# Optimization experiments

Measured on AMD Instinct MI355X. Metric: run time of the kernel, lower is better.

Reference implementation:

```python
import jax, jax.numpy as jnp
import numpy as np

B, T, IN, HID, BR, OUT = 128, 250, 700, 1024, 4, 20
VTH1, VTH2, DT = 0.5, 0.5, 1.0

# heaviside spike with multi-gaussian surrogate grad (DH-SNN ActFun_adp)
@jax.custom_vjp
def spike_fn(v):
    return (v > 0).astype(v.dtype)

def _spike_fwd(v):
    return spike_fn(v), v

def _spike_bwd(v, g):
    gamma, lens, scale, hight = 0.5, 0.5, 6.0, 0.15
    def gauss(x, mu, sigma):
        return jnp.exp(-((x - mu) ** 2) / (2.0 * sigma ** 2)) / (jnp.sqrt(2.0 * jnp.pi) * sigma)
    sg = (gauss(v, 0.0, lens) * (1.0 + hight)
          - gauss(v, lens, scale * lens) * hight
          - gauss(v, -lens, scale * lens) * hight)
    return (g * sg * gamma,)

spike_fn.defvjp(_spike_fwd, _spike_bwd)

def _make_mask(rng):
    # each output neuron's BR branches see disjoint equal slices of a random permutation
    K = IN + HID  # pad == 0 since (IN+HID) % BR == 0
    seg = K // BR
    mask = np.zeros((HID * BR, K), dtype=np.int32)
    for i in range(HID):
        seq = rng.permutation(K)
        for j in range(BR):
            mask[i * BR + j, seq[j * seg:(j + 1) * seg]] = 1
    return mask

def setup_inputs() -> dict:
    key = jax.random.key(0)
    ks = jax.random.split(key, 10)
    K = IN + HID
    x = jax.random.uniform(ks[0], (B, T, IN), dtype=jnp.float32)
    W1 = jax.random.normal(ks[1], (HID * BR, K), dtype=jnp.float32) / jnp.sqrt(jnp.float32(K))
    b1 = jnp.zeros((HID * BR,), jnp.float32)
    tau_m1 = jax.random.uniform(ks[2], (HID,), jnp.float32, 0.0, 4.0)
    tau_n = jax.random.uniform(ks[3], (HID, BR), jnp.float32, 0.0, 4.0)
    W2 = jax.random.normal(ks[4], (OUT, HID), dtype=jnp.float32) / jnp.sqrt(jnp.float32(HID))
    b2 = jnp.zeros((OUT,), jnp.float32)
    tau_m2 = jax.random.uniform(ks[5], (OUT,), jnp.float32, 0.0, 4.0)
    mem1_0 = jax.random.uniform(ks[6], (B, HID), jnp.float32)
    mem2_0 = jax.random.uniform(ks[7], (B, OUT), jnp.float32)
    mask = jnp.asarray(_make_mask(np.random.default_rng(0)))
    return dict(x=x, W1=W1, b1=b1, tau_m1=tau_m1, tau_n=tau_n, W2=W2, b2=b2,
                tau_m2=tau_m2, mem1_0=mem1_0, mem2_0=mem2_0, mask=mask)

def reference(x, W1, b1, tau_m1, tau_n, W2, b2, tau_m2, mem1_0, mem2_0, mask):
    bsz = x.shape[0]
    W1m = W1 * mask.astype(W1.dtype)  # branch-sparse dendritic weights
    alpha1 = jax.nn.sigmoid(tau_m1)   # [HID]
    beta = jax.nn.sigmoid(tau_n)      # [HID, BR]
    alpha2 = jax.nn.sigmoid(tau_m2)   # [OUT]
    spk1_0 = jnp.zeros((bsz, HID), x.dtype)
    d0 = jnp.zeros((bsz, HID, BR), x.dtype)
    spk2_0 = jnp.zeros((bsz, OUT), x.dtype)

    def step(carry, x_t):
        mem1, spk1, d_inp, mem2, spk2 = carry
        k_in = jnp.concatenate([x_t, spk1], axis=1)          # [B, IN+HID]
        ff = (k_in @ W1m.T + b1).reshape(bsz, HID, BR)       # dendritic branch input
        d_inp = beta * d_inp + (1.0 - beta) * ff             # per-branch decay
        l_in = d_inp.sum(axis=2)                             # [B, HID]
        mem1 = mem1 * alpha1 + (1.0 - alpha1) * l_in - VTH1 * spk1 * DT
        spk1 = spike_fn(mem1 - VTH1)
        d2 = spk1 @ W2.T + b2
        mem2 = mem2 * alpha2 + (1.0 - alpha2) * d2 - VTH2 * spk2 * DT
        spk2 = spike_fn(mem2 - VTH2)
        out = jax.nn.log_softmax(mem2, axis=1)
        return (mem1, spk1, d_inp, mem2, spk2), out

    _, ys = jax.lax.scan(step, (mem1_0, spk1_0, d0, mem2_0, spk2_0), jnp.swapaxes(x, 0, 1))
    return jnp.transpose(ys, (1, 2, 0))  # [B, OUT, T]
```

## Files before the change

### kernel.cpp

```cpp
#include <hip/hip_runtime.h>
#include <stdint.h>

#define BATCH 128
#define TSTEPS 250
#define NIN 700
#define NHID 1024
#define NBR 4
#define NOUT 20
#define KDIM 1724
#define NR 4096
#define VTH 0.5f


__global__ void setup_small(const float* __restrict__ tau_m1, const float* __restrict__ tau_n,
                            const float* __restrict__ tau_m2, const float* __restrict__ W2,
                            float* __restrict__ alpha1, float* __restrict__ beta,
                            float* __restrict__ alpha2, float* __restrict__ W2T) {
    int i = blockIdx.x * blockDim.x + threadIdx.x;
    if (i < NHID)  alpha1[i] = 1.f / (1.f + expf(-tau_m1[i]));
    if (i < NR)    beta[i]   = 1.f / (1.f + expf(-tau_n[i]));
    if (i < 32)    alpha2[i] = (i < NOUT) ? 1.f / (1.f + expf(-tau_m2[i])) : 0.f;
    if (i < NHID * 32) {
        int j = i >> 5, o = i & 31;
        W2T[i] = (o < NOUT) ? W2[o * NHID + j] : 0.f;
    }
}

__global__ void setup_weights(const float* __restrict__ W1, const int* __restrict__ mask,
                              float* __restrict__ W1xT, float* __restrict__ W1hTb) {
    const int total1 = NIN * NR;
    const int total2 = 256 * 16384;
    for (int i = blockIdx.x * blockDim.x + threadIdx.x; i < total1 + total2;
         i += gridDim.x * blockDim.x) {
        if (i < total1) {
            int k = i >> 12, r = i & 4095;
            size_t src = (size_t)r * KDIM + k;
            W1xT[i] = W1[src] * (float)mask[src];
        } else {
            int j = i - total1;
            int blk = j >> 14, rem = j & 16383;
            int n = rem >> 4, rl = rem & 15;
            int r = (blk << 4) + rl;
            size_t src = (size_t)r * KDIM + NIN + n;
            W1hTb[j] = W1[src] * (float)mask[src];
        }
    }
}

__global__ void init_state(const float* __restrict__ mem1_0, const float* __restrict__ mem2_0,
                           float* __restrict__ mem1, float* __restrict__ mem2,
                           float* __restrict__ spk2, float* __restrict__ d_inp,
                           uint32_t* __restrict__ spkg, uint32_t* __restrict__ cnt) {
    int i = blockIdx.x * blockDim.x + threadIdx.x;
    if (i < BATCH * NR) d_inp[i] = 0.f;
    if (i < BATCH * NHID) mem1[i] = mem1_0[i];
    if (i < BATCH * NOUT) { mem2[i] = mem2_0[i]; spk2[i] = 0.f; }
    if (i < 8192) spkg[i] = 0u;
    if (i == 0) cnt[0] = 0u;
}


#define GBM 128
#define GBN 128
#define GBK 16

__global__ __launch_bounds__(256) void ffx_gemm(const float* __restrict__ x,
                                                const float* __restrict__ W1xT,
                                                const float* __restrict__ b1,
                                                float* __restrict__ ffx, int t0) {
    __shared__ float As[GBK][GBM];
    __shared__ float Bs[GBK][GBN];
    int dt = blockIdx.x, bn = blockIdx.y;
    int tid = threadIdx.x;
    int tn = tid & 15, tm = tid >> 4;

    float acc[8][8];
#pragma unroll
    for (int i = 0; i < 8; ++i)
#pragma unroll
        for (int j = 0; j < 8; ++j) acc[i][j] = 0.f;

    int m_l = tid >> 1;
    const float* xrow = x + ((size_t)m_l * TSTEPS + t0 + dt) * NIN;
    int kh = (tid & 1) * 8;
    int kb = tid >> 4;
    int nb = (tid & 15) * 8;

    for (int k0 = 0; k0 < NIN; k0 += GBK) {
        float av[8];
#pragma unroll
        for (int u = 0; u < 8; ++u) {
            int k = k0 + kh + u;
            av[u] = (k < NIN) ? xrow[k] : 0.f;
        }
#pragma unroll
        for (int u = 0; u < 8; ++u) As[kh + u][m_l] = av[u];

        bool kok = (k0 + kb) < NIN;
        const float* bp = W1xT + (size_t)(k0 + kb) * NR + bn * GBN + nb;
        float bv[8];
#pragma unroll
        for (int u = 0; u < 8; ++u) bv[u] = kok ? bp[u] : 0.f;
#pragma unroll
        for (int u = 0; u < 8; ++u) Bs[kb][nb + u] = bv[u];

        __syncthreads();
#pragma unroll
        for (int kk = 0; kk < GBK; ++kk) {
            float a[8], b[8];
#pragma unroll
            for (int u = 0; u < 8; ++u) a[u] = As[kk][tm * 8 + u];
#pragma unroll
            for (int u = 0; u < 8; ++u) b[u] = Bs[kk][tn * 8 + u];
#pragma unroll
            for (int i = 0; i < 8; ++i)
#pragma unroll
                for (int j = 0; j < 8; ++j) acc[i][j] += a[i] * b[j];
        }
        __syncthreads();
    }

    float bias[8];
#pragma unroll
    for (int j = 0; j < 8; ++j) bias[j] = b1[bn * GBN + tn * 8 + j];
#pragma unroll
    for (int i = 0; i < 8; ++i) {
        int brow = tm * 8 + i;
        float* cp = ffx + ((size_t)dt * BATCH + brow) * NR + bn * GBN + tn * 8;
#pragma unroll
        for (int j = 0; j < 8; ++j) cp[j] = acc[i][j] + bias[j];
    }
}


__global__ __launch_bounds__(1024) void persist2(
    const float* __restrict__ alpha1, const float* __restrict__ beta,
    const float* __restrict__ alpha2, float* __restrict__ mem1,
    float* __restrict__ mem2, float* __restrict__ spk2,
    float* __restrict__ d_inp, const float* __restrict__ W1hTb,
    const float* __restrict__ W2T, const float* __restrict__ ffx,
    const float* __restrict__ b2v, float* __restrict__ out,
    uint32_t* __restrict__ spkg, uint32_t* __restrict__ cnt,
    int t0, int tc, int last, int epoch0) {
    __shared__ float lds_W[NHID * 17];
    __shared__ uint32_t lds_spk[4096];
    __shared__ uint32_t lds_mask[128 * 33];

    const int blk = blockIdx.x;
    const int tid = threadIdx.x;

    {
        const float4* wsrc = (const float4*)(W1hTb + (size_t)blk * 16384);
        for (int i4 = tid; i4 < 4096; i4 += 1024) {
            float4 v = wsrc[i4];
            int n = i4 >> 2, rb = (i4 & 3) * 4;
            lds_W[n * 17 + rb + 0] = v.x;
            lds_W[n * 17 + rb + 1] = v.y;
            lds_W[n * 17 + rb + 2] = v.z;
            lds_W[n * 17 + rb + 3] = v.w;
        }
    }

    const int r_l = tid & 15;
    const int bg  = tid >> 4;
    const int r_g = (blk << 4) + r_l;
    const int neuron = (blk << 2) + (r_l >> 2);
    const float beta_r = beta[r_g];
    const float al = alpha1[neuron];
    const int b0 = bg * 2, b1 = bg * 2 + 1;

    float di0 = d_inp[(size_t)b0 * NR + r_g];
    float di1 = d_inp[(size_t)b1 * NR + r_g];
    float mm0 = mem1[b0 * NHID + neuron];
    float mm1 = mem1[b1 * NHID + neuron];

    const int o2 = tid & 31;
    const int sub = tid >> 5;
    const bool l2blk = (blk < 16) && ((sub & 3) == 0);
    const int b2b = (blk << 3) + (sub >> 2);
    float m2 = 0.f, s2v = 0.f, a2 = 0.f, bo = 0.f;
    if (l2blk && o2 < NOUT) {
        a2 = alpha2[o2];
        bo = b2v[o2];
        m2 = mem2[b2b * NOUT + o2];
        s2v = spk2[b2b * NOUT + o2];
    }

    const int iters = tc + (last ? 1 : 0);
    for (int it = 0; it < iters; ++it) {
        const int tt = t0 + it;

        float ff0 = 0.f, ff1 = 0.f;
        if (tt < TSTEPS) {
            const float* fr = ffx + (size_t)it * ((size_t)BATCH * NR);
            ff0 = fr[(size_t)b0 * NR + r_g];
            ff1 = fr[(size_t)b1 * NR + r_g];
        }

        {
            const uint32_t* spg = spkg + (size_t)((tt + 1) & 1) * 4096;
#pragma unroll
            for (int k = 0; k < 4; ++k) {
                int idx = tid + (k << 10);
                lds_spk[idx ^ ((idx >> 7) & 31)] =
                    __hip_atomic_load(&spg[idx], __ATOMIC_RELAXED, __HIP_MEMORY_SCOPE_AGENT);
            }
        }
        __syncthreads();

        {
            const int w = tid & 31;
            const int bq = tid >> 5;
            const int g = bq >> 1;
            uint32_t sw[8];
#pragma unroll
            for (int m = 0; m < 8; ++m) {
                int raw = (w << 7) + (m << 4) + g;
                sw[m] = lds_spk[raw ^ (w & 31)];
            }
#pragma unroll
            for (int u = 0; u < 4; ++u) {
                const int b = (bq << 2) + u;
                const int j = ((bq & 1) << 2) + u;
                uint32_t word = 0;
#pragma unroll
                for (int m = 0; m < 8; ++m)
                    word |= ((sw[m] >> (j << 2)) & 0xFu) << (m << 2);
                lds_mask[b * 33 + w] = word;
            }
        }
        __syncthreads();

        uint32_t* spn = spkg + (size_t)(tt & 1) * 4096;

        if (tt < TSTEPS) {
            const uint32_t* mw0 = &lds_mask[b0 * 33];
            const uint32_t* mw1 = &lds_mask[b1 * 33];
            float acc0 = 0.f, acc1 = 0.f;
            for (int w = 0; w < 32; ++w) {
                uint32_t bits0 = mw0[w];
                while (bits0) {
                    int p = __builtin_ctz(bits0);
                    bits0 &= bits0 - 1;
                    acc0 += lds_W[((w << 5) + p) * 17 + r_l];
                }
                uint32_t bits1 = mw1[w];
                while (bits1) {
                    int p = __builtin_ctz(bits1);
                    bits1 &= bits1 - 1;
                    acc1 += lds_W[((w << 5) + p) * 17 + r_l];
                }
            }
            di0 = beta_r * di0 + (1.f - beta_r) * (acc0 + ff0);
            di1 = beta_r * di1 + (1.f - beta_r) * (acc1 + ff1);
            float ls0 = di0 + __shfl_xor(di0, 1); ls0 += __shfl_xor(ls0, 2);
            float ls1 = di1 + __shfl_xor(di1, 1); ls1 += __shfl_xor(ls1, 2);
            float sp0 = (float)((mw0[neuron >> 5] >> (neuron & 31)) & 1u);
            float sp1 = (float)((mw1[neuron >> 5] >> (neuron & 31)) & 1u);
            float mn0 = mm0 * al + (1.f - al) * ls0 - VTH * sp0;  mm0 = mn0;
            float mn1 = mm1 * al + (1.f - al) * ls1 - VTH * sp1;  mm1 = mn1;
            bool sk0 = (mn0 - VTH) > 0.f;
            bool sk1 = (mn1 - VTH) > 0.f;
            unsigned long long bal0 = __ballot(sk0 && ((r_l & 3) == 0));
            unsigned long long bal1 = __ballot(sk1 && ((r_l & 3) == 0));
            uint32_t dw = 0;
#pragma unroll
            for (int q = 0; q < 4; ++q) {
                uint32_t nb0 = (uint32_t)((bal0 >> (q * 16)) & 1ull)
                             | ((uint32_t)((bal0 >> (q * 16 + 4)) & 1ull) << 1)
                             | ((uint32_t)((bal0 >> (q * 16 + 8)) & 1ull) << 2)
                             | ((uint32_t)((bal0 >> (q * 16 + 12)) & 1ull) << 3);
                uint32_t nb1 = (uint32_t)((bal1 >> (q * 16)) & 1ull)
                             | ((uint32_t)((bal1 >> (q * 16 + 4)) & 1ull) << 1)
                             | ((uint32_t)((bal1 >> (q * 16 + 8)) & 1ull) << 2)
                             | ((uint32_t)((bal1 >> (q * 16 + 12)) & 1ull) << 3);
                dw |= (nb0 << (q * 8)) | (nb1 << (q * 8 + 4));
            }
            if ((tid & 63) == 0)
                __hip_atomic_store(&spn[(blk << 4) + (tid >> 6)], dw, __ATOMIC_RELAXED,
                                   __HIP_MEMORY_SCOPE_AGENT);
        }

        if (tt > 0 && l2blk) {
            const uint32_t* mw = &lds_mask[b2b * 33];
            float d2 = bo;
            for (int w = 0; w < 32; ++w) {
                uint32_t bits = mw[w];
                while (bits) {
                    int p = __builtin_ctz(bits);
                    bits &= bits - 1;
                    d2 += W2T[(((w << 5) + p) << 5) + o2];
                }
            }
            float m2n = m2 * a2 + (1.f - a2) * d2 - VTH * s2v;
            m2 = m2n;
            s2v = ((m2n - VTH) > 0.f) ? 1.f : 0.f;
            float v = (o2 < NOUT) ? m2n : -3.4e38f;
#pragma unroll
            for (int off = 16; off >= 1; off >>= 1) v = fmaxf(v, __shfl_xor(v, off, 32));
            float e = (o2 < NOUT) ? expf(m2n - v) : 0.f;
            float s = e;
#pragma unroll
            for (int off = 16; off >= 1; off >>= 1) s += __shfl_xor(s, off, 32);
            if (o2 < NOUT) out[((size_t)b2b * NOUT + o2) * TSTEPS + (tt - 1)] = (m2n - v) - logf(s);
        }

        if (it + 1 < iters) {
            __syncthreads();
            if (tid == 0) {
                __hip_atomic_fetch_add(cnt, 1u, __ATOMIC_RELEASE, __HIP_MEMORY_SCOPE_AGENT);
                uint32_t tgt = 256u * (uint32_t)(epoch0 + it + 1);
                while (__hip_atomic_load(cnt, __ATOMIC_RELAXED, __HIP_MEMORY_SCOPE_AGENT) < tgt)
                    __builtin_amdgcn_s_sleep(2);
            }
            __syncthreads();
        }
    }

    d_inp[(size_t)b0 * NR + r_g] = di0;
    d_inp[(size_t)b1 * NR + r_g] = di1;
    if ((r_l & 3) == 0) {
        mem1[b0 * NHID + neuron] = mm0;
        mem1[b1 * NHID + neuron] = mm1;
    }
    if (l2blk && o2 < NOUT) {
        mem2[b2b * NOUT + o2] = m2;
        spk2[b2b * NOUT + o2] = s2v;
    }
}


extern "C" void kernel_launch(void* const* d_in, const int* in_sizes, int n_in,
                              void* d_out, int out_size, void* d_ws, size_t ws_size,
                              hipStream_t stream) {
    const float* x      = (const float*)d_in[0];
    const float* W1     = (const float*)d_in[1];
    const float* b1     = (const float*)d_in[2];
    const float* tau_m1 = (const float*)d_in[3];
    const float* tau_n  = (const float*)d_in[4];
    const float* W2     = (const float*)d_in[5];
    const float* b2     = (const float*)d_in[6];
    const float* tau_m2 = (const float*)d_in[7];
    const float* mem1_0 = (const float*)d_in[8];
    const float* mem2_0 = (const float*)d_in[9];
    const int*   mask   = (const int*)d_in[10];
    float* out = (float*)d_out;

    float* ws = (float*)d_ws;
    size_t F = 0;
    float* alpha1 = ws + F; F += 1024;
    float* beta   = ws + F; F += 4096;
    float* alpha2 = ws + F; F += 32;
    float* mem1   = ws + F; F += BATCH * NHID;
    float* mem2   = ws + F; F += BATCH * NOUT;
    float* spk2   = ws + F; F += BATCH * NOUT;
    float* d_inp  = ws + F; F += BATCH * NR;
    float* W1xT   = ws + F; F += (size_t)NIN * NR;
    float* W1hTb  = ws + F; F += (size_t)256 * 16384;
    float* W2T    = ws + F; F += NHID * 32;
    uint32_t* spkg = (uint32_t*)(ws + F); F += 2 * BATCH * 64;
    uint32_t* cnt  = (uint32_t*)(ws + F); F += 64;
    float* ffx = ws + F;

    size_t ws_f = ws_size / 4;
    size_t avail = (ws_f > F) ? (ws_f - F) : 0;
    size_t per_t = (size_t)BATCH * NR;
    int Tc = (int)(avail / per_t);
    if (Tc < 1) Tc = 1;
    if (Tc > TSTEPS) Tc = TSTEPS;

    hipLaunchKernelGGL(setup_small, dim3(128), dim3(256), 0, stream,
                       tau_m1, tau_n, tau_m2, W2, alpha1, beta, alpha2, W2T);
    hipLaunchKernelGGL(setup_weights, dim3(2048), dim3(256), 0, stream, W1, mask, W1xT, W1hTb);
    hipLaunchKernelGGL(init_state, dim3(2048), dim3(256), 0, stream,
                       mem1_0, mem2_0, mem1, mem2, spk2, d_inp, spkg, cnt);

    int chunk_start = 0;
    int barriers_done = 0;
    while (chunk_start < TSTEPS) {
        int tc = TSTEPS - chunk_start;
        if (tc > Tc) tc = Tc;
        int last = (chunk_start + tc >= TSTEPS) ? 1 : 0;

        hipLaunchKernelGGL(ffx_gemm, dim3(tc, 32), dim3(256), 0, stream,
                           x, W1xT, b1, ffx, chunk_start);
        hipLaunchKernelGGL(persist2, dim3(256), dim3(1024), 0, stream,
                           alpha1, beta, alpha2, mem1, mem2, spk2, d_inp, W1hTb, W2T,
                           ffx, b2, out, spkg, cnt, chunk_start, tc, last, barriers_done);

        int iters = tc + (last ? 1 : 0);
        barriers_done += iters - 1;
        chunk_start += tc;
    }
}
```

Baseline: 7.089 ms.

## Replace global counter barrier with per-timestep per-block spike flags

The single atomic-counter grid barrier between timesteps is replaced by per-timestep, per-block ready flags with release/acquire semantics. Spike words now go into a per-timestep buffer rather than a double buffer, so each block waits only until all 256 producer flags for its step are set and never spins on one contended counter. The layer-2 readout is also split across 32 blocks with an 8-way partial-sum reduction in LDS, replacing 16 blocks that each did a serial loop. This costs more workspace for the spike and flag arrays and adds extra __syncthreads inside the step loop.

```diff
diff --git a/kernel.cpp b/kernel.cpp
--- a/kernel.cpp
+++ b/kernel.cpp
@@ -50,13 +50,13 @@
 __global__ void init_state(const float* __restrict__ mem1_0, const float* __restrict__ mem2_0,
                            float* __restrict__ mem1, float* __restrict__ mem2,
                            float* __restrict__ spk2, float* __restrict__ d_inp,
-                           uint32_t* __restrict__ spkg, uint32_t* __restrict__ cnt) {
+                           uint32_t* __restrict__ spkdat, uint32_t* __restrict__ spkseq) {
     int i = blockIdx.x * blockDim.x + threadIdx.x;
     if (i < BATCH * NR) d_inp[i] = 0.f;
     if (i < BATCH * NHID) mem1[i] = mem1_0[i];
     if (i < BATCH * NOUT) { mem2[i] = mem2_0[i]; spk2[i] = 0.f; }
-    if (i < 8192) spkg[i] = 0u;
-    if (i == 0) cnt[0] = 0u;
+    if (i < 4096) spkdat[i] = 0u;
+    if (i < (TSTEPS + 1) * 256) spkseq[i] = (i < 256) ? 1u : 0u;
 }
 
 
@@ -133,15 +133,15 @@
 }
 
 
-__global__ __launch_bounds__(1024) void persist2(
+__global__ __launch_bounds__(1024) void persist3(
     const float* __restrict__ alpha1, const float* __restrict__ beta,
     const float* __restrict__ alpha2, float* __restrict__ mem1,
     float* __restrict__ mem2, float* __restrict__ spk2,
     float* __restrict__ d_inp, const float* __restrict__ W1hTb,
     const float* __restrict__ W2T, const float* __restrict__ ffx,
     const float* __restrict__ b2v, float* __restrict__ out,
-    uint32_t* __restrict__ spkg, uint32_t* __restrict__ cnt,
-    int t0, int tc, int last, int epoch0) {
+    uint32_t* __restrict__ spkdat, uint32_t* __restrict__ spkseq,
+    int t0, int tc, int last) {
     __shared__ float lds_W[NHID * 17];
     __shared__ uint32_t lds_spk[4096];
     __shared__ uint32_t lds_mask[128 * 33];
@@ -176,19 +176,30 @@
 
     const int o2 = tid & 31;
     const int sub = tid >> 5;
-    const bool l2blk = (blk < 16) && ((sub & 3) == 0);
-    const int b2b = (blk << 3) + (sub >> 2);
+    const bool l2red = (blk < 32) && ((sub & 7) == 0);
+    const int b2b = (blk << 2) + (sub >> 3);
     float m2 = 0.f, s2v = 0.f, a2 = 0.f, bo = 0.f;
-    if (l2blk && o2 < NOUT) {
+    if (l2red && o2 < NOUT) {
         a2 = alpha2[o2];
         bo = b2v[o2];
         m2 = mem2[b2b * NOUT + o2];
         s2v = spk2[b2b * NOUT + o2];
     }
+    float* lds_f = (float*)lds_spk;
 
     const int iters = tc + (last ? 1 : 0);
     for (int it = 0; it < iters; ++it) {
         const int tt = t0 + it;
+
+        {
+            const uint32_t* fl = spkseq + (size_t)tt * 256;
+            if (tid < 256) {
+                while (__hip_atomic_load(fl + tid, __ATOMIC_ACQUIRE,
+                                         __HIP_MEMORY_SCOPE_AGENT) == 0u)
+                    __builtin_amdgcn_s_sleep(1);
+            }
+            __syncthreads();
+        }
 
         float ff0 = 0.f, ff1 = 0.f;
         if (tt < TSTEPS) {
@@ -198,7 +209,7 @@
         }
 
         {
-            const uint32_t* spg = spkg + (size_t)((tt + 1) & 1) * 4096;
+            const uint32_t* spg = spkdat + (size_t)tt * 4096;
 #pragma unroll
             for (int k = 0; k < 4; ++k) {
                 int idx = tid + (k << 10);
@@ -231,9 +242,8 @@
         }
         __syncthreads();
 
-        uint32_t* spn = spkg + (size_t)(tt & 1) * 4096;
-
         if (tt < TSTEPS) {
+            uint32_t* spn = spkdat + (size_t)(tt + 1) * 4096;
             const uint32_t* mw0 = &lds_mask[b0 * 33];
             const uint32_t* mw1 = &lds_mask[b1 * 33];
             float acc0 = 0.f, acc1 = 0.f;
@@ -281,17 +291,32 @@
                                    __HIP_MEMORY_SCOPE_AGENT);
         }
 
-        if (tt > 0 && l2blk) {
-            const uint32_t* mw = &lds_mask[b2b * 33];
-            float d2 = bo;
-            for (int w = 0; w < 32; ++w) {
+        __syncthreads();
+        if (tt < TSTEPS && tid == 0)
+            __hip_atomic_store(&spkseq[(size_t)(tt + 1) * 256 + blk], 1u,
+                               __ATOMIC_RELEASE, __HIP_MEMORY_SCOPE_AGENT);
+
+        if (tt > 0 && blk < 32) {
+            const int bp = (blk << 2) + (sub >> 3);
+            const int q = sub & 7;
+            const uint32_t* mw = &lds_mask[bp * 33];
+            float part = 0.f;
+#pragma unroll
+            for (int w = q * 4; w < q * 4 + 4; ++w) {
                 uint32_t bits = mw[w];
                 while (bits) {
                     int p = __builtin_ctz(bits);
                     bits &= bits - 1;
-                    d2 += W2T[(((w << 5) + p) << 5) + o2];
+                    part += W2T[(((w << 5) + p) << 5) + o2];
                 }
             }
+            lds_f[(sub << 5) + o2] = part;
+        }
+        if (blk < 32) __syncthreads();
+        if (tt > 0 && l2red) {
+            float d2 = bo;
+#pragma unroll
+            for (int j = 0; j < 8; ++j) d2 += lds_f[((sub + j) << 5) + o2];
             float m2n = m2 * a2 + (1.f - a2) * d2 - VTH * s2v;
             m2 = m2n;
             s2v = ((m2n - VTH) > 0.f) ? 1.f : 0.f;
@@ -303,17 +328,6 @@
 #pragma unroll
             for (int off = 16; off >= 1; off >>= 1) s += __shfl_xor(s, off, 32);
             if (o2 < NOUT) out[((size_t)b2b * NOUT + o2) * TSTEPS + (tt - 1)] = (m2n - v) - logf(s);
-        }
-
-        if (it + 1 < iters) {
-            __syncthreads();
-            if (tid == 0) {
-                __hip_atomic_fetch_add(cnt, 1u, __ATOMIC_RELEASE, __HIP_MEMORY_SCOPE_AGENT);
-                uint32_t tgt = 256u * (uint32_t)(epoch0 + it + 1);
-                while (__hip_atomic_load(cnt, __ATOMIC_RELAXED, __HIP_MEMORY_SCOPE_AGENT) < tgt)
-                    __builtin_amdgcn_s_sleep(2);
-            }
-            __syncthreads();
         }
     }
 
@@ -323,7 +337,7 @@
         mem1[b0 * NHID + neuron] = mm0;
         mem1[b1 * NHID + neuron] = mm1;
     }
-    if (l2blk && o2 < NOUT) {
+    if (l2red && o2 < NOUT) {
         mem2[b2b * NOUT + o2] = m2;
         spk2[b2b * NOUT + o2] = s2v;
     }
@@ -358,8 +372,8 @@
     float* W1xT   = ws + F; F += (size_t)NIN * NR;
     float* W1hTb  = ws + F; F += (size_t)256 * 16384;
     float* W2T    = ws + F; F += NHID * 32;
-    uint32_t* spkg = (uint32_t*)(ws + F); F += 2 * BATCH * 64;
-    uint32_t* cnt  = (uint32_t*)(ws + F); F += 64;
+    uint32_t* spkdat = (uint32_t*)(ws + F); F += (size_t)(TSTEPS + 1) * 4096;
+    uint32_t* spkseq = (uint32_t*)(ws + F); F += (size_t)(TSTEPS + 1) * 256;
     float* ffx = ws + F;
 
     size_t ws_f = ws_size / 4;
@@ -373,10 +387,9 @@
                        tau_m1, tau_n, tau_m2, W2, alpha1, beta, alpha2, W2T);
     hipLaunchKernelGGL(setup_weights, dim3(2048), dim3(256), 0, stream, W1, mask, W1xT, W1hTb);
     hipLaunchKernelGGL(init_state, dim3(2048), dim3(256), 0, stream,
-                       mem1_0, mem2_0, mem1, mem2, spk2, d_inp, spkg, cnt);
+                       mem1_0, mem2_0, mem1, mem2, spk2, d_inp, spkdat, spkseq);
 
     int chunk_start = 0;
-    int barriers_done = 0;
     while (chunk_start < TSTEPS) {
         int tc = TSTEPS - chunk_start;
         if (tc > Tc) tc = Tc;
@@ -384,12 +397,10 @@
 
         hipLaunchKernelGGL(ffx_gemm, dim3(tc, 32), dim3(256), 0, stream,
                            x, W1xT, b1, ffx, chunk_start);
-        hipLaunchKernelGGL(persist2, dim3(256), dim3(1024), 0, stream,
+        hipLaunchKernelGGL(persist3, dim3(256), dim3(1024), 0, stream,
                            alpha1, beta, alpha2, mem1, mem2, spk2, d_inp, W1hTb, W2T,
-                           ffx, b2, out, spkg, cnt, chunk_start, tc, last, barriers_done);
-
-        int iters = tc + (last ? 1 : 0);
-        barriers_done += iters - 1;
+                           ffx, b2, out, spkdat, spkseq, chunk_start, tc, last);
+
         chunk_start += tc;
     }
 }
```

After: 9.953 ms. 1.4x slower.

## Replace flat grid barrier with hierarchical split-phase barrier overlapping layer-2 work

Applied to the files above, without the earlier changes.

The single global counter that all 256 blocks incremented and spun on is replaced by a two-level barrier. Blocks arrive on one of 16 group counters, and the last arriver of each group bumps a top counter. Arrival now happens before the layer-2 readout and log-softmax, and the wait is moved to the start of the next iteration, so the readout overlaps the barrier latency. The intent is to cut atomic contention on one address and hide sync time, at the cost of more complex epoch arithmetic that must stay correct across chunked launches.

```diff
diff --git a/kernel.cpp b/kernel.cpp
--- a/kernel.cpp
+++ b/kernel.cpp
@@ -50,13 +50,13 @@
 __global__ void init_state(const float* __restrict__ mem1_0, const float* __restrict__ mem2_0,
                            float* __restrict__ mem1, float* __restrict__ mem2,
                            float* __restrict__ spk2, float* __restrict__ d_inp,
-                           uint32_t* __restrict__ spkg, uint32_t* __restrict__ cnt) {
+                           uint32_t* __restrict__ spkg, uint32_t* __restrict__ bar) {
     int i = blockIdx.x * blockDim.x + threadIdx.x;
     if (i < BATCH * NR) d_inp[i] = 0.f;
     if (i < BATCH * NHID) mem1[i] = mem1_0[i];
     if (i < BATCH * NOUT) { mem2[i] = mem2_0[i]; spk2[i] = 0.f; }
     if (i < 8192) spkg[i] = 0u;
-    if (i == 0) cnt[0] = 0u;
+    if (i < 1024) bar[i] = 0u;
 }
 
 
@@ -133,14 +133,14 @@
 }
 
 
-__global__ __launch_bounds__(1024) void persist2(
+__global__ __launch_bounds__(1024) void persist4(
     const float* __restrict__ alpha1, const float* __restrict__ beta,
     const float* __restrict__ alpha2, float* __restrict__ mem1,
     float* __restrict__ mem2, float* __restrict__ spk2,
     float* __restrict__ d_inp, const float* __restrict__ W1hTb,
     const float* __restrict__ W2T, const float* __restrict__ ffx,
     const float* __restrict__ b2v, float* __restrict__ out,
-    uint32_t* __restrict__ spkg, uint32_t* __restrict__ cnt,
+    uint32_t* __restrict__ spkg, uint32_t* __restrict__ bar,
     int t0, int tc, int last, int epoch0) {
     __shared__ float lds_W[NHID * 17];
     __shared__ uint32_t lds_spk[4096];
@@ -186,6 +186,8 @@
         s2v = spk2[b2b * NOUT + o2];
     }
 
+    uint32_t* grp = bar + 32 + ((blk & 15) << 5);
+
     const int iters = tc + (last ? 1 : 0);
     for (int it = 0; it < iters; ++it) {
         const int tt = t0 + it;
@@ -197,6 +199,16 @@
             ff1 = fr[(size_t)b1 * NR + r_g];
         }
 
+        if (it > 0) {
+            if (tid == 0) {
+                uint32_t tgt = 16u * (uint32_t)(epoch0 + it);
+                while (__hip_atomic_load(&bar[0], __ATOMIC_RELAXED,
+                                         __HIP_MEMORY_SCOPE_AGENT) < tgt)
+                    __builtin_amdgcn_s_sleep(2);
+            }
+            __syncthreads();
+        }
+
         {
             const uint32_t* spg = spkg + (size_t)((tt + 1) & 1) * 4096;
 #pragma unroll
@@ -231,9 +243,8 @@
         }
         __syncthreads();
 
-        uint32_t* spn = spkg + (size_t)(tt & 1) * 4096;
-
         if (tt < TSTEPS) {
+            uint32_t* spn = spkg + (size_t)(tt & 1) * 4096;
             const uint32_t* mw0 = &lds_mask[b0 * 33];
             const uint32_t* mw1 = &lds_mask[b1 * 33];
             float acc0 = 0.f, acc1 = 0.f;
@@ -281,6 +292,16 @@
                                    __HIP_MEMORY_SCOPE_AGENT);
         }
 
+        __syncthreads();
+        if (it + 1 < iters && tid == 0) {
+            uint32_t e16 = 16u * (uint32_t)(epoch0 + it + 1);
+            uint32_t old = __hip_atomic_fetch_add(grp, 1u, __ATOMIC_RELEASE,
+                                                  __HIP_MEMORY_SCOPE_AGENT);
+            if (old == e16 - 1u)
+                __hip_atomic_fetch_add(&bar[0], 1u, __ATOMIC_RELEASE,
+                                       __HIP_MEMORY_SCOPE_AGENT);
+        }
+
         if (tt > 0 && l2blk) {
             const uint32_t* mw = &lds_mask[b2b * 33];
             float d2 = bo;
@@ -303,17 +324,6 @@
 #pragma unroll
             for (int off = 16; off >= 1; off >>= 1) s += __shfl_xor(s, off, 32);
             if (o2 < NOUT) out[((size_t)b2b * NOUT + o2) * TSTEPS + (tt - 1)] = (m2n - v) - logf(s);
-        }
-
-        if (it + 1 < iters) {
-            __syncthreads();
-            if (tid == 0) {
-                __hip_atomic_fetch_add(cnt, 1u, __ATOMIC_RELEASE, __HIP_MEMORY_SCOPE_AGENT);
-                uint32_t tgt = 256u * (uint32_t)(epoch0 + it + 1);
-                while (__hip_atomic_load(cnt, __ATOMIC_RELAXED, __HIP_MEMORY_SCOPE_AGENT) < tgt)
-                    __builtin_amdgcn_s_sleep(2);
-            }
-            __syncthreads();
         }
     }
 
@@ -358,8 +368,8 @@
     float* W1xT   = ws + F; F += (size_t)NIN * NR;
     float* W1hTb  = ws + F; F += (size_t)256 * 16384;
     float* W2T    = ws + F; F += NHID * 32;
-    uint32_t* spkg = (uint32_t*)(ws + F); F += 2 * BATCH * 64;
-    uint32_t* cnt  = (uint32_t*)(ws + F); F += 64;
+    uint32_t* spkg = (uint32_t*)(ws + F); F += 8192;
+    uint32_t* bar  = (uint32_t*)(ws + F); F += 1024;
     float* ffx = ws + F;
 
     size_t ws_f = ws_size / 4;
@@ -373,7 +383,7 @@
                        tau_m1, tau_n, tau_m2, W2, alpha1, beta, alpha2, W2T);
     hipLaunchKernelGGL(setup_weights, dim3(2048), dim3(256), 0, stream, W1, mask, W1xT, W1hTb);
     hipLaunchKernelGGL(init_state, dim3(2048), dim3(256), 0, stream,
-                       mem1_0, mem2_0, mem1, mem2, spk2, d_inp, spkg, cnt);
+                       mem1_0, mem2_0, mem1, mem2, spk2, d_inp, spkg, bar);
 
     int chunk_start = 0;
     int barriers_done = 0;
@@ -384,9 +394,9 @@
 
         hipLaunchKernelGGL(ffx_gemm, dim3(tc, 32), dim3(256), 0, stream,
                            x, W1xT, b1, ffx, chunk_start);
-        hipLaunchKernelGGL(persist2, dim3(256), dim3(1024), 0, stream,
+        hipLaunchKernelGGL(persist4, dim3(256), dim3(1024), 0, stream,
                            alpha1, beta, alpha2, mem1, mem2, spk2, d_inp, W1hTb, W2T,
-                           ffx, b2, out, spkg, cnt, chunk_start, tc, last, barriers_done);
+                           ffx, b2, out, spkg, bar, chunk_start, tc, last, barriers_done);
 
         int iters = tc + (last ? 1 : 0);
         barriers_done += iters - 1;
```

After: 7.415 ms. 1.05x slower.

## Compute recurrent spike-weight product with bf16 MFMA using hi/lo split weights

Applied to the files above, without the earlier changes.

Replaces the per-thread bit-scan gather over LDS weights in the persistent recurrent kernel with MFMA 16x16x32 bf16 matrix ops. Spike bits become 0/1 bf16 A-fragments, and the masked recurrent weights are stored as a bf16 high part plus a bf16 residual so the product stays close to fp32. The grid barrier is also split: blocks signal arrival after publishing spikes and wait only at the start of the next step, so the layer-2 output work overlaps the barrier. This adds double the MFMA work for the hi/lo split and extra LDS partial-sum buffers with an additional syncthreads per step.

```diff
diff --git a/kernel.cpp b/kernel.cpp
--- a/kernel.cpp
+++ b/kernel.cpp
@@ -10,6 +10,9 @@
 #define KDIM 1724
 #define NR 4096
 #define VTH 0.5f
+
+typedef float f32x4 __attribute__((ext_vector_type(4)));
+typedef short s16x8 __attribute__((ext_vector_type(8)));
 
 
 __global__ void setup_small(const float* __restrict__ tau_m1, const float* __restrict__ tau_n,
@@ -26,8 +29,14 @@
     }
 }
 
+__device__ __forceinline__ uint16_t f2bf_rne(float x) {
+    uint32_t u = __float_as_uint(x);
+    return (uint16_t)((u + 0x7FFFu + ((u >> 16) & 1u)) >> 16);
+}
+
 __global__ void setup_weights(const float* __restrict__ W1, const int* __restrict__ mask,
-                              float* __restrict__ W1xT, float* __restrict__ W1hTb) {
+                              float* __restrict__ W1xT, uint16_t* __restrict__ fragH,
+                              uint16_t* __restrict__ fragL) {
     const int total1 = NIN * NR;
     const int total2 = 256 * 16384;
     for (int i = blockIdx.x * blockDim.x + threadIdx.x; i < total1 + total2;
@@ -37,12 +46,16 @@
             size_t src = (size_t)r * KDIM + k;
             W1xT[i] = W1[src] * (float)mask[src];
         } else {
-            int j = i - total1;
-            int blk = j >> 14, rem = j & 16383;
-            int n = rem >> 4, rl = rem & 15;
-            int r = (blk << 4) + rl;
-            size_t src = (size_t)r * KDIM + NIN + n;
-            W1hTb[j] = W1[src] * (float)mask[src];
+            int j2 = i - total1;
+            int j = j2 & 7, lane = (j2 >> 3) & 63, ks = (j2 >> 9) & 31, blk = j2 >> 14;
+            int k = ks * 32 + ((lane >> 4) & 3) * 8 + j;
+            int r = blk * 16 + (lane & 15);
+            size_t src = (size_t)r * KDIM + NIN + k;
+            float w = W1[src] * (float)mask[src];
+            uint16_t hb = f2bf_rne(w);
+            float hf = __uint_as_float((uint32_t)hb << 16);
+            fragH[j2] = hb;
+            fragL[j2] = f2bf_rne(w - hf);
         }
     }
 }
@@ -133,46 +146,53 @@
 }
 
 
-__global__ __launch_bounds__(1024) void persist2(
+__global__ __launch_bounds__(1024) void persist5(
     const float* __restrict__ alpha1, const float* __restrict__ beta,
     const float* __restrict__ alpha2, float* __restrict__ mem1,
     float* __restrict__ mem2, float* __restrict__ spk2,
-    float* __restrict__ d_inp, const float* __restrict__ W1hTb,
-    const float* __restrict__ W2T, const float* __restrict__ ffx,
-    const float* __restrict__ b2v, float* __restrict__ out,
-    uint32_t* __restrict__ spkg, uint32_t* __restrict__ cnt,
-    int t0, int tc, int last, int epoch0) {
-    __shared__ float lds_W[NHID * 17];
+    float* __restrict__ d_inp, const uint16_t* __restrict__ fragH_g,
+    const uint16_t* __restrict__ fragL_g, const float* __restrict__ W2T,
+    const float* __restrict__ ffx, const float* __restrict__ b2v,
+    float* __restrict__ out, uint32_t* __restrict__ spkg,
+    uint32_t* __restrict__ cnt, int t0, int tc, int last, int epoch0) {
+    __shared__ __align__(16) uint16_t lds_fh[16384];
+    __shared__ __align__(16) uint16_t lds_fl[16384];
     __shared__ uint32_t lds_spk[4096];
     __shared__ uint32_t lds_mask[128 * 33];
+    __shared__ float lds_part[2048];
+    __shared__ float lds_part2[2048];
 
     const int blk = blockIdx.x;
     const int tid = threadIdx.x;
+    const int l   = tid & 63;
+    const int wv  = tid >> 6;
 
     {
-        const float4* wsrc = (const float4*)(W1hTb + (size_t)blk * 16384);
-        for (int i4 = tid; i4 < 4096; i4 += 1024) {
-            float4 v = wsrc[i4];
-            int n = i4 >> 2, rb = (i4 & 3) * 4;
-            lds_W[n * 17 + rb + 0] = v.x;
-            lds_W[n * 17 + rb + 1] = v.y;
-            lds_W[n * 17 + rb + 2] = v.z;
-            lds_W[n * 17 + rb + 3] = v.w;
-        }
-    }
-
-    const int r_l = tid & 15;
-    const int bg  = tid >> 4;
-    const int r_g = (blk << 4) + r_l;
-    const int neuron = (blk << 2) + (r_l >> 2);
-    const float beta_r = beta[r_g];
-    const float al = alpha1[neuron];
-    const int b0 = bg * 2, b1 = bg * 2 + 1;
-
-    float di0 = d_inp[(size_t)b0 * NR + r_g];
-    float di1 = d_inp[(size_t)b1 * NR + r_g];
-    float mm0 = mem1[b0 * NHID + neuron];
-    float mm1 = mem1[b1 * NHID + neuron];
+        const float4* sH = (const float4*)(fragH_g + (size_t)blk * 16384);
+        const float4* sL = (const float4*)(fragL_g + (size_t)blk * 16384);
+        for (int i4 = tid; i4 < 2048; i4 += 1024) {
+            ((float4*)lds_fh)[i4] = sH[i4];
+            ((float4*)lds_fl)[i4] = sL[i4];
+        }
+    }
+
+    const int mt = wv & 7;
+    const int kh = wv >> 3;
+    const int arow = mt * 16 + (l & 15);
+    const int ksl = ((l >> 4) & 3) * 8;
+
+    const int ub    = tid >> 3;
+    const int unrn  = (tid >> 1) & 3;
+    const int uhalf = tid & 1;
+    const int nrn_g = (blk << 2) + unrn;
+    const int rl0   = unrn * 4 + uhalf * 2;
+    const int r_g0  = (blk << 4) + rl0;
+    const float bet0 = beta[r_g0];
+    const float bet1 = beta[r_g0 + 1];
+    const float al   = alpha1[nrn_g];
+    float di0 = d_inp[(size_t)ub * NR + r_g0];
+    float di1 = d_inp[(size_t)ub * NR + r_g0 + 1];
+    float mm  = mem1[ub * NHID + nrn_g];
 
     const int o2 = tid & 31;
     const int sub = tid >> 5;
@@ -192,9 +212,18 @@
 
         float ff0 = 0.f, ff1 = 0.f;
         if (tt < TSTEPS) {
-            const float* fr = ffx + (size_t)it * ((size_t)BATCH * NR);
-            ff0 = fr[(size_t)b0 * NR + r_g];
-            ff1 = fr[(size_t)b1 * NR + r_g];
+            const float2 fv = *(const float2*)(ffx + (size_t)it * (BATCH * NR)
+                                               + (size_t)ub * NR + r_g0);
+            ff0 = fv.x; ff1 = fv.y;
+        }
+
+        if (it > 0) {
+            if (tid == 0) {
+                uint32_t tgt = 256u * (uint32_t)(epoch0 + it);
+                while (__hip_atomic_load(cnt, __ATOMIC_RELAXED, __HIP_MEMORY_SCOPE_AGENT) < tgt)
+                    __builtin_amdgcn_s_sleep(2);
+            }
+            __syncthreads();
         }
 
         {
@@ -231,55 +260,59 @@
         }
         __syncthreads();
 
-        uint32_t* spn = spkg + (size_t)(tt & 1) * 4096;
-
         if (tt < TSTEPS) {
-            const uint32_t* mw0 = &lds_mask[b0 * 33];
-            const uint32_t* mw1 = &lds_mask[b1 * 33];
-            float acc0 = 0.f, acc1 = 0.f;
-            for (int w = 0; w < 32; ++w) {
-                uint32_t bits0 = mw0[w];
-                while (bits0) {
-                    int p = __builtin_ctz(bits0);
-                    bits0 &= bits0 - 1;
-                    acc0 += lds_W[((w << 5) + p) * 17 + r_l];
+            f32x4 acc = {0.f, 0.f, 0.f, 0.f};
+            const int maskbase = arow * 33;
+#pragma unroll 4
+            for (int i = 0; i < 16; ++i) {
+                const int ks = kh * 16 + i;
+                uint32_t bits = (lds_mask[maskbase + ks] >> ksl) & 0xFFu;
+                union { uint32_t u[4]; s16x8 v; } a;
+                a.u[0] = ((bits & 1u)  ? 0x3F80u : 0u) | ((bits & 2u)   ? 0x3F800000u : 0u);
+                a.u[1] = ((bits & 4u)  ? 0x3F80u : 0u) | ((bits & 8u)   ? 0x3F800000u : 0u);
+                a.u[2] = ((bits & 16u) ? 0x3F80u : 0u) | ((bits & 32u)  ? 0x3F800000u : 0u);
+                a.u[3] = ((bits & 64u) ? 0x3F80u : 0u) | ((bits & 128u) ? 0x3F800000u : 0u);
+                const s16x8 bh = *(const s16x8*)&lds_fh[(ks * 64 + l) * 8];
+                const s16x8 bl = *(const s16x8*)&lds_fl[(ks * 64 + l) * 8];
+                acc = __builtin_amdgcn_mfma_f32_16x16x32_bf16(a.v, bh, acc, 0, 0, 0);
+                acc = __builtin_amdgcn_mfma_f32_16x16x32_bf16(a.v, bl, acc, 0, 0, 0);
+            }
+            float* pp = (kh == 0 ? lds_part : lds_part2)
+                        + ((mt * 16 + (l & 15)) * 16 + ((l >> 4) & 3) * 4);
+            *(float4*)pp = *(float4*)&acc;
+        }
+        __syncthreads();
+
+        if (tt < TSTEPS) {
+            const int pb = ((ub >> 4) * 16 + rl0) * 16 + (ub & 15);
+            float s0 = lds_part[pb]      + lds_part2[pb];
+            float s1 = lds_part[pb + 16] + lds_part2[pb + 16];
+            di0 = bet0 * di0 + (1.f - bet0) * (s0 + ff0);
+            di1 = bet1 * di1 + (1.f - bet1) * (s1 + ff1);
+            float t2 = di0 + di1;
+            float lsum = t2 + __shfl_xor(t2, 1);
+            float sp_prev = (float)((lds_mask[ub * 33 + (nrn_g >> 5)] >> (nrn_g & 31)) & 1u);
+            float mn = mm * al + (1.f - al) * lsum - VTH * sp_prev;
+            mm = mn;
+            bool spk = (mn - VTH) > 0.f;
+            unsigned long long bal = __ballot(spk && (uhalf == 0));
+            if (l == 0) {
+                uint32_t dw = 0;
+#pragma unroll
+                for (int j = 0; j < 8; ++j) {
+                    uint32_t v = (uint32_t)(bal >> (j * 8)) & 0x55u;
+                    uint32_t nib = (v & 1u) | ((v >> 1) & 2u) | ((v >> 2) & 4u) | ((v >> 3) & 8u);
+                    dw |= nib << (4 * j);
                 }
-                uint32_t bits1 = mw1[w];
-                while (bits1) {
-                    int p = __builtin_ctz(bits1);
-                    bits1 &= bits1 - 1;
-                    acc1 += lds_W[((w << 5) + p) * 17 + r_l];
-                }
-            }
-            di0 = beta_r * di0 + (1.f - beta_r) * (acc0 + ff0);
-            di1 = beta_r * di1 + (1.f - beta_r) * (acc1 + ff1);
-            float ls0 = di0 + __shfl_xor(di0, 1); ls0 += __shfl_xor(ls0, 2);
-            float ls1 = di1 + __shfl_xor(di1, 1); ls1 += __shfl_xor(ls1, 2);
-            float sp0 = (float)((mw0[neuron >> 5] >> (neuron & 31)) & 1u);
-            float sp1 = (float)((mw1[neuron >> 5] >> (neuron & 31)) & 1u);
-            float mn0 = mm0 * al + (1.f - al) * ls0 - VTH * sp0;  mm0 = mn0;
-            float mn1 = mm1 * al + (1.f - al) * ls1 - VTH * sp1;  mm1 = mn1;
-            bool sk0 = (mn0 - VTH) > 0.f;
-            bool sk1 = (mn1 - VTH) > 0.f;
-            unsigned long long bal0 = __ballot(sk0 && ((r_l & 3) == 0));
-            unsigned long long bal1 = __ballot(sk1 && ((r_l & 3) == 0));
-            uint32_t dw = 0;
-#pragma unroll
-            for (int q = 0; q < 4; ++q) {
-                uint32_t nb0 = (uint32_t)((bal0 >> (q * 16)) & 1ull)
-                             | ((uint32_t)((bal0 >> (q * 16 + 4)) & 1ull) << 1)
-                             | ((uint32_t)((bal0 >> (q * 16 + 8)) & 1ull) << 2)
-                             | ((uint32_t)((bal0 >> (q * 16 + 12)) & 1ull) << 3);
-                uint32_t nb1 = (uint32_t)((bal1 >> (q * 16)) & 1ull)
-                             | ((uint32_t)((bal1 >> (q * 16 + 4)) & 1ull) << 1)
-                             | ((uint32_t)((bal1 >> (q * 16 + 8)) & 1ull) << 2)
-                             | ((uint32_t)((bal1 >> (q * 16 + 12)) & 1ull) << 3);
-                dw |= (nb0 << (q * 8)) | (nb1 << (q * 8 + 4));
-            }
-            if ((tid & 63) == 0)
-                __hip_atomic_store(&spn[(blk << 4) + (tid >> 6)], dw, __ATOMIC_RELAXED,
+                uint32_t* spn = spkg + (size_t)(tt & 1) * 4096;
+                __hip_atomic_store(&spn[(blk << 4) + wv], dw, __ATOMIC_RELAXED,
                                    __HIP_MEMORY_SCOPE_AGENT);
-        }
+            }
+        }
+
+        __syncthreads();
+        if (it + 1 < iters && tid == 0)
+            __hip_atomic_fetch_add(cnt, 1u, __ATOMIC_RELEASE, __HIP_MEMORY_SCOPE_AGENT);
 
         if (tt > 0 && l2blk) {
             const uint32_t* mw = &lds_mask[b2b * 33];
@@ -304,25 +337,11 @@
             for (int off = 16; off >= 1; off >>= 1) s += __shfl_xor(s, off, 32);
             if (o2 < NOUT) out[((size_t)b2b * NOUT + o2) * TSTEPS + (tt - 1)] = (m2n - v) - logf(s);
         }
-
-        if (it + 1 < iters) {
-            __syncthreads();
-            if (tid == 0) {
-                __hip_atomic_fetch_add(cnt, 1u, __ATOMIC_RELEASE, __HIP_MEMORY_SCOPE_AGENT);
-                uint32_t tgt = 256u * (uint32_t)(epoch0 + it + 1);
-                while (__hip_atomic_load(cnt, __ATOMIC_RELAXED, __HIP_MEMORY_SCOPE_AGENT) < tgt)
-                    __builtin_amdgcn_s_sleep(2);
-            }
-            __syncthreads();
-        }
-    }
-
-    d_inp[(size_t)b0 * NR + r_g] = di0;
-    d_inp[(size_t)b1 * NR + r_g] = di1;
-    if ((r_l & 3) == 0) {
-        mem1[b0 * NHID + neuron] = mm0;
-        mem1[b1 * NHID + neuron] = mm1;
-    }
+    }
+
+    d_inp[(size_t)ub * NR + r_g0]     = di0;
+    d_inp[(size_t)ub * NR + r_g0 + 1] = di1;
+    if (uhalf == 0) mem1[ub * NHID + nrn_g] = mm;
     if (l2blk && o2 < NOUT) {
         mem2[b2b * NOUT + o2] = m2;
         spk2[b2b * NOUT + o2] = s2v;
@@ -356,9 +375,10 @@
     float* spk2   = ws + F; F += BATCH * NOUT;
     float* d_inp  = ws + F; F += BATCH * NR;
     float* W1xT   = ws + F; F += (size_t)NIN * NR;
-    float* W1hTb  = ws + F; F += (size_t)256 * 16384;
+    uint16_t* fragH = (uint16_t*)(ws + F); F += (size_t)256 * 16384 / 2;
+    uint16_t* fragL = (uint16_t*)(ws + F); F += (size_t)256 * 16384 / 2;
     float* W2T    = ws + F; F += NHID * 32;
-    uint32_t* spkg = (uint32_t*)(ws + F); F += 2 * BATCH * 64;
+    uint32_t* spkg = (uint32_t*)(ws + F); F += 8192;
     uint32_t* cnt  = (uint32_t*)(ws + F); F += 64;
     float* ffx = ws + F;
 
@@ -371,7 +391,8 @@
 
     hipLaunchKernelGGL(setup_small, dim3(128), dim3(256), 0, stream,
                        tau_m1, tau_n, tau_m2, W2, alpha1, beta, alpha2, W2T);
-    hipLaunchKernelGGL(setup_weights, dim3(2048), dim3(256), 0, stream, W1, mask, W1xT, W1hTb);
+    hipLaunchKernelGGL(setup_weights, dim3(2048), dim3(256), 0, stream,
+                       W1, mask, W1xT, fragH, fragL);
     hipLaunchKernelGGL(init_state, dim3(2048), dim3(256), 0, stream,
                        mem1_0, mem2_0, mem1, mem2, spk2, d_inp, spkg, cnt);
 
@@ -384,9 +405,9 @@
 
         hipLaunchKernelGGL(ffx_gemm, dim3(tc, 32), dim3(256), 0, stream,
                            x, W1xT, b1, ffx, chunk_start);
-        hipLaunchKernelGGL(persist2, dim3(256), dim3(1024), 0, stream,
-                           alpha1, beta, alpha2, mem1, mem2, spk2, d_inp, W1hTb, W2T,
-                           ffx, b2, out, spkg, cnt, chunk_start, tc, last, barriers_done);
+        hipLaunchKernelGGL(persist5, dim3(256), dim3(1024), 0, stream,
+                           alpha1, beta, alpha2, mem1, mem2, spk2, d_inp, fragH, fragL,
+                           W2T, ffx, b2, out, spkg, cnt, chunk_start, tc, last, barriers_done);
 
         int iters = tc + (last ? 1 : 0);
         barriers_done += iters - 1;
```

Result: slower. 8.003 ms (+12.9%).
